# Performance work log

Hardware: AMD Instinct MI355X
Metric: run time of the kernel (lower is better)

The kernel has to match this reference:

```python
import jax, jax.numpy as jnp
import numpy as np

N = 10000
E = 320000


def spmm(edge_row, edge_col, edge_val, h):
    # out[i] = sum_{e: row[e]==i} val[e] * h[col[e]]  (sparse adjacency @ h)
    msgs = edge_val[:, None] * h[edge_col]          # [E, d]
    return jax.ops.segment_sum(msgs, edge_row, num_segments=N)


def setup_inputs() -> dict:
    key = jax.random.key(0)
    ks = jax.random.split(key, 8)
    x = jax.random.normal(ks[0], (N, 128), dtype=jnp.float32)
    edge_row = jax.random.randint(ks[1], (E,), 0, N, dtype=jnp.int32)
    edge_col = jax.random.randint(ks[2], (E,), 0, N, dtype=jnp.int32)
    edge_val = jax.random.uniform(ks[3], (E,), dtype=jnp.float32)
    # Xavier-uniform-ish init as in the torch module: U(-1/sqrt(fan_out), 1/sqrt(fan_out))
    def w(k, fi, fo):
        s = 1.0 / np.sqrt(fo)
        return jax.random.uniform(k, (fi, fo), minval=-s, maxval=s, dtype=jnp.float32)
    W0 = w(ks[4], 128, 128)
    W1 = w(ks[5], 128, 128)
    W2 = w(ks[6], 128, 64)
    Wb = w(ks[7], 64, 64)
    return {"x": x, "edge_row": edge_row, "edge_col": edge_col, "edge_val": edge_val,
            "W0": W0, "W1": W1, "W2": W2, "Wb": Wb}


def reference(x, edge_row, edge_col, edge_val, W0, W1, W2, Wb):
    h = x
    for W in (W0, W1, W2):
        h = jax.nn.elu(spmm(edge_row, edge_col, edge_val, h @ W))
        # dropout is inactive in eval mode (training=False)
    S = (Wb + Wb.T) * 0.5                          # symmetric [d, d]
    out = jax.nn.sigmoid(h @ (S @ h.T))            # [N, N]
    return out
```

## Files before the change

### kernel.cpp

```cpp
#include <hip/hip_runtime.h>
#include <hip/hip_bf16.h>
#include <math.h>

typedef short short8 __attribute__((ext_vector_type(8)));
typedef short short4v __attribute__((ext_vector_type(4)));
typedef float f32x4 __attribute__((ext_vector_type(4)));

__device__ inline void bsplit(float x, short& h, short& l) {
    __hip_bfloat16 hb = __float2bfloat16(x);
    float hf = __bfloat162float(hb);
    __hip_bfloat16 lb = __float2bfloat16(x - hf);
    h = *reinterpret_cast<short*>(&hb);
    l = *reinterpret_cast<short*>(&lb);
}


__global__ void zero_i32(int* __restrict__ p, int n) {
    int i = blockIdx.x * blockDim.x + threadIdx.x;
    if (i < n) p[i] = 0;
}

__global__ void hist_kernel(const int* __restrict__ row, int* __restrict__ hist, int E) {
    int i = blockIdx.x * blockDim.x + threadIdx.x;
    if (i < E) atomicAdd(&hist[row[i]], 1);
}

__global__ void scan_kernel(const int* __restrict__ hist, int* __restrict__ rowptr,
                            int* __restrict__ cursor, int n) {
    __shared__ int wsum[16];
    __shared__ int carry_s;
    int tid = threadIdx.x, lane = tid & 63, wid = tid >> 6;
    if (tid == 0) { carry_s = 0; rowptr[0] = 0; }
    __syncthreads();
    for (int base = 0; base < n; base += 1024) {
        int idx = base + tid;
        int v = (idx < n) ? hist[idx] : 0;
        int x = v;
#pragma unroll
        for (int d = 1; d < 64; d <<= 1) {
            int t = __shfl_up(x, d, 64);
            if (lane >= d) x += t;
        }
        if (lane == 63) wsum[wid] = x;
        __syncthreads();
        if (wid == 0) {
            int s = (lane < 16) ? wsum[lane] : 0;
#pragma unroll
            for (int d = 1; d < 16; d <<= 1) {
                int t = __shfl_up(s, d, 64);
                if (lane >= d) s += t;
            }
            if (lane < 16) wsum[lane] = s;
        }
        __syncthreads();
        int woff = (wid > 0) ? wsum[wid - 1] : 0;
        int inc = x + woff + carry_s;
        if (idx < n) {
            rowptr[idx + 1] = inc;
            cursor[idx] = inc - v;
        }
        __syncthreads();
        if (tid == 1023) carry_s = inc;
        __syncthreads();
    }
}

__global__ void scatter_kernel(const int* __restrict__ row, const int* __restrict__ col,
                               const float* __restrict__ val, int* __restrict__ cursor,
                               int* __restrict__ colsort, float* __restrict__ valsort, int E) {
    int i = blockIdx.x * blockDim.x + threadIdx.x;
    if (i < E) {
        int r = row[i];
        int p = atomicAdd(&cursor[r], 1);
        colsort[p] = col[i];
        valsort[p] = val[i];
    }
}

template <int K, int M>
__global__ void gemm_layer(const float* __restrict__ A, const float* __restrict__ W,
                           float* __restrict__ out, int n) {
    __shared__ float a[8 * K];
    int j = threadIdx.x;
    int row0 = blockIdx.x * 8;
    constexpr int K4 = K / 4;
    for (int idx = j; idx < 8 * K4; idx += M) {
        int r = idx / K4, k4 = idx % K4;
        float4 v = make_float4(0.f, 0.f, 0.f, 0.f);
        if (row0 + r < n) v = *reinterpret_cast<const float4*>(A + (long)(row0 + r) * K + k4 * 4);
        *reinterpret_cast<float4*>(a + r * K + k4 * 4) = v;
    }
    __syncthreads();
    float acc[8] = {0, 0, 0, 0, 0, 0, 0, 0};
#pragma unroll 8
    for (int k = 0; k < K; k++) {
        float w = W[k * M + j];
#pragma unroll
        for (int r = 0; r < 8; r++) acc[r] += a[r * K + k] * w;
    }
#pragma unroll
    for (int r = 0; r < 8; r++) {
        if (row0 + r < n) out[(long)(row0 + r) * M + j] = acc[r];
    }
}

__global__ void gemm_head(const float* __restrict__ A, const float* __restrict__ S,
                          short* __restrict__ Th, short* __restrict__ Tl, int n) {
    __shared__ float a[8 * 64];
    int j = threadIdx.x;
    int row0 = blockIdx.x * 8;
    for (int idx = j; idx < 8 * 16; idx += 64) {
        int r = idx >> 4, k4 = idx & 15;
        float4 v = make_float4(0.f, 0.f, 0.f, 0.f);
        if (row0 + r < n) v = *reinterpret_cast<const float4*>(A + (long)(row0 + r) * 64 + k4 * 4);
        *reinterpret_cast<float4*>(a + r * 64 + k4 * 4) = v;
    }
    __syncthreads();
    float acc[8] = {0, 0, 0, 0, 0, 0, 0, 0};
#pragma unroll 8
    for (int k = 0; k < 64; k++) {
        float w = S[k * 64 + j];
#pragma unroll
        for (int r = 0; r < 8; r++) acc[r] += a[r * 64 + k] * w;
    }
#pragma unroll
    for (int r = 0; r < 8; r++) {
        if (row0 + r < n) {
            short h, l;
            bsplit(acc[r], h, l);
            Th[(long)(row0 + r) * 64 + j] = h;
            Tl[(long)(row0 + r) * 64 + j] = l;
        }
    }
}

template <int D>
__global__ void spmm_elu_v2(const int* __restrict__ rowptr, const int* __restrict__ cols,
                            const float* __restrict__ vals, const float* __restrict__ hw,
                            float* __restrict__ out, int n) {
    constexpr int LPR = D / 4;
    constexpr int EPI = 64 / LPR;
    int wave = (blockIdx.x * blockDim.x + threadIdx.x) >> 6;
    int lane = threadIdx.x & 63;
    if (wave >= n) return;
    int sub = lane % LPR, grp = lane / LPR;
    int s = rowptr[wave], e = rowptr[wave + 1];
    float ax = 0.f, ay = 0.f, az = 0.f, aw = 0.f;
    int pe = s + grp;
    int c = 0; float v = 0.f;
    if (pe < e) { c = cols[pe]; v = vals[pe]; }
    for (int p = s; p < e; p += EPI) {
        int pn = p + EPI + grp;
        int cn = 0; float vn = 0.f;
        if (pn < e) { cn = cols[pn]; vn = vals[pn]; }
        float4 h4 = *reinterpret_cast<const float4*>(hw + (long)c * D + sub * 4);
        ax += v * h4.x; ay += v * h4.y; az += v * h4.z; aw += v * h4.w;
        c = cn; v = vn;
    }
#pragma unroll
    for (int m = LPR; m < 64; m <<= 1) {
        ax += __shfl_xor(ax, m, 64);
        ay += __shfl_xor(ay, m, 64);
        az += __shfl_xor(az, m, 64);
        aw += __shfl_xor(aw, m, 64);
    }
    if (grp == 0) {
        float4 o;
        o.x = ax > 0.f ? ax : (__expf(ax) - 1.f);
        o.y = ay > 0.f ? ay : (__expf(ay) - 1.f);
        o.z = az > 0.f ? az : (__expf(az) - 1.f);
        o.w = aw > 0.f ? aw : (__expf(aw) - 1.f);
        *reinterpret_cast<float4*>(out + (long)wave * D + sub * 4) = o;
    }
}

__global__ void spmm_elu_split64(const int* __restrict__ rowptr, const int* __restrict__ cols,
                                 const float* __restrict__ vals, const float* __restrict__ hw,
                                 float* __restrict__ h3, short* __restrict__ Hh,
                                 short* __restrict__ Hl, int n) {
    constexpr int D = 64, LPR = 16, EPI = 4;
    int wave = (blockIdx.x * blockDim.x + threadIdx.x) >> 6;
    int lane = threadIdx.x & 63;
    if (wave >= n) return;
    int sub = lane % LPR, grp = lane / LPR;
    int s = rowptr[wave], e = rowptr[wave + 1];
    float ax = 0.f, ay = 0.f, az = 0.f, aw = 0.f;
    int pe = s + grp;
    int c = 0; float v = 0.f;
    if (pe < e) { c = cols[pe]; v = vals[pe]; }
    for (int p = s; p < e; p += EPI) {
        int pn = p + EPI + grp;
        int cn = 0; float vn = 0.f;
        if (pn < e) { cn = cols[pn]; vn = vals[pn]; }
        float4 h4 = *reinterpret_cast<const float4*>(hw + (long)c * D + sub * 4);
        ax += v * h4.x; ay += v * h4.y; az += v * h4.z; aw += v * h4.w;
        c = cn; v = vn;
    }
#pragma unroll
    for (int m = LPR; m < 64; m <<= 1) {
        ax += __shfl_xor(ax, m, 64);
        ay += __shfl_xor(ay, m, 64);
        az += __shfl_xor(az, m, 64);
        aw += __shfl_xor(aw, m, 64);
    }
    if (grp == 0) {
        float4 o;
        o.x = ax > 0.f ? ax : (__expf(ax) - 1.f);
        o.y = ay > 0.f ? ay : (__expf(ay) - 1.f);
        o.z = az > 0.f ? az : (__expf(az) - 1.f);
        o.w = aw > 0.f ? aw : (__expf(aw) - 1.f);
        *reinterpret_cast<float4*>(h3 + (long)wave * D + sub * 4) = o;
        short4v hs, ls;
        short t0, t1, t2, t3, u0, u1, u2, u3;
        bsplit(o.x, t0, u0);
        bsplit(o.y, t1, u1);
        bsplit(o.z, t2, u2);
        bsplit(o.w, t3, u3);
        hs[0] = t0; hs[1] = t1; hs[2] = t2; hs[3] = t3;
        ls[0] = u0; ls[1] = u1; ls[2] = u2; ls[3] = u3;
        *reinterpret_cast<short4v*>(Hh + (long)wave * D + sub * 4) = hs;
        *reinterpret_cast<short4v*>(Hl + (long)wave * D + sub * 4) = ls;
    }
}

__global__ void sym_kernel(const float* __restrict__ Wb, float* __restrict__ S) {
    int i = blockIdx.x * blockDim.x + threadIdx.x;
    if (i < 64 * 64) {
        int r = i >> 6, c = i & 63;
        S[i] = 0.5f * (Wb[r * 64 + c] + Wb[c * 64 + r]);
    }
}

__global__ void pad_zero(short* __restrict__ Th, short* __restrict__ Tl,
                         short* __restrict__ Hh, short* __restrict__ Hl,
                         int startRow, int padRows) {
    int i = blockIdx.x * blockDim.x + threadIdx.x;
    int tot = padRows * 64;
    if (i < tot) {
        long off = (long)startRow * 64 + i;
        Th[off] = 0; Tl[off] = 0; Hh[off] = 0; Hl[off] = 0;
    }
}

__global__ __launch_bounds__(256) void final_mfma(
    const short* __restrict__ Th, const short* __restrict__ Tl,
    const short* __restrict__ Hh, const short* __restrict__ Hl,
    float* __restrict__ out, int n) {
    int tid = threadIdx.x;
    int wave = tid >> 6, lane = tid & 63;
    int row0 = blockIdx.y * 128 + (wave >> 1) * 64;
    int col0 = blockIdx.x * 128 + (wave & 1) * 64;
    int lrow = lane & 15;
    int koff = (lane >> 4) * 8;

    const short* ThB = Th + (long)(row0 + lrow) * 64 + koff;
    const short* TlB = Tl + (long)(row0 + lrow) * 64 + koff;
    const short* HhB = Hh + (long)(col0 + lrow) * 64 + koff;
    const short* HlB = Hl + (long)(col0 + lrow) * 64 + koff;

    f32x4 acc[4][4];
#pragma unroll
    for (int r = 0; r < 4; r++)
#pragma unroll
        for (int c = 0; c < 4; c++) acc[r][c] = (f32x4){0.f, 0.f, 0.f, 0.f};

#pragma unroll
    for (int ks = 0; ks < 2; ks++) {
        int kb = ks * 32;
        short8 ah[4], bh[4], al[4], bl[4];
#pragma unroll
        for (int r = 0; r < 4; r++) ah[r] = *reinterpret_cast<const short8*>(ThB + (long)(r * 16) * 64 + kb);
#pragma unroll
        for (int c = 0; c < 4; c++) bh[c] = *reinterpret_cast<const short8*>(HhB + (long)(c * 16) * 64 + kb);
#pragma unroll
        for (int r = 0; r < 4; r++) al[r] = *reinterpret_cast<const short8*>(TlB + (long)(r * 16) * 64 + kb);
#pragma unroll
        for (int c = 0; c < 4; c++) bl[c] = *reinterpret_cast<const short8*>(HlB + (long)(c * 16) * 64 + kb);

#pragma unroll
        for (int r = 0; r < 4; r++)
#pragma unroll
            for (int c = 0; c < 4; c++)
                acc[r][c] = __builtin_amdgcn_mfma_f32_16x16x32_bf16(ah[r], bh[c], acc[r][c], 0, 0, 0);
#pragma unroll
        for (int r = 0; r < 4; r++)
#pragma unroll
            for (int c = 0; c < 4; c++)
                acc[r][c] = __builtin_amdgcn_mfma_f32_16x16x32_bf16(ah[r], bl[c], acc[r][c], 0, 0, 0);
#pragma unroll
        for (int r = 0; r < 4; r++)
#pragma unroll
            for (int c = 0; c < 4; c++)
                acc[r][c] = __builtin_amdgcn_mfma_f32_16x16x32_bf16(al[r], bh[c], acc[r][c], 0, 0, 0);
    }

    int orow = (lane >> 4) * 4;
    bool full = (row0 + 64 <= n) && (col0 + 64 <= n);
    if (full) {
#pragma unroll
        for (int r = 0; r < 4; r++) {
#pragma unroll
            for (int q = 0; q < 4; q++) {
                long base = (long)(row0 + r * 16 + orow + q) * n + col0 + lrow;
#pragma unroll
                for (int c = 0; c < 4; c++) {
                    float x = acc[r][c][q];
                    out[base + c * 16] = __builtin_amdgcn_rcpf(1.f + __expf(-x));
                }
            }
        }
    } else {
#pragma unroll
        for (int r = 0; r < 4; r++) {
#pragma unroll
            for (int q = 0; q < 4; q++) {
                int i = row0 + r * 16 + orow + q;
                if (i < n) {
#pragma unroll
                    for (int c = 0; c < 4; c++) {
                        int j = col0 + c * 16 + lrow;
                        if (j < n) {
                            float x = acc[r][c][q];
                            out[(long)i * n + j] = __builtin_amdgcn_rcpf(1.f + __expf(-x));
                        }
                    }
                }
            }
        }
    }
}

extern "C" void kernel_launch(void* const* d_in, const int* in_sizes, int n_in,
                              void* d_out, int out_size, void* d_ws, size_t ws_size,
                              hipStream_t stream) {
    const float* x    = (const float*)d_in[0];
    const int*   erow = (const int*)d_in[1];
    const int*   ecol = (const int*)d_in[2];
    const float* eval = (const float*)d_in[3];
    const float* W0   = (const float*)d_in[4];
    const float* W1   = (const float*)d_in[5];
    const float* W2   = (const float*)d_in[6];
    const float* Wb   = (const float*)d_in[7];
    float* out = (float*)d_out;

    int N = in_sizes[0] / 128;
    int E = in_sizes[1];
    int G = (N + 127) / 128;
    int Npad = G * 128;

    char* w = (char*)d_ws;
    size_t off = 0;
    auto alloc = [&](size_t bytes) -> void* {
        void* p = w + off;
        off += (bytes + 255) & ~(size_t)255;
        return p;
    };
    float* bufA    = (float*)alloc((size_t)N * 128 * 4);
    float* bufB    = (float*)alloc((size_t)N * 128 * 4);
    float* h3      = (float*)alloc((size_t)N * 64 * 4);
    float* S       = (float*)alloc(64 * 64 * 4);
    int*   colsort = (int*)alloc((size_t)E * 4);
    float* valsort = (float*)alloc((size_t)E * 4);
    int*   rowptr  = (int*)alloc((size_t)(N + 1) * 4);
    int*   cursor  = (int*)alloc((size_t)N * 4);
    int*   hist    = (int*)alloc((size_t)N * 4);
    short* Th      = (short*)alloc((size_t)Npad * 64 * 2);
    short* Tl      = (short*)alloc((size_t)Npad * 64 * 2);
    short* Hh      = (short*)alloc((size_t)Npad * 64 * 2);
    short* Hl      = (short*)alloc((size_t)Npad * 64 * 2);

    zero_i32<<<(N + 255) / 256, 256, 0, stream>>>(hist, N);
    hist_kernel<<<(E + 255) / 256, 256, 0, stream>>>(erow, hist, E);
    scan_kernel<<<1, 1024, 0, stream>>>(hist, rowptr, cursor, N);
    scatter_kernel<<<(E + 255) / 256, 256, 0, stream>>>(erow, ecol, eval, cursor, colsort, valsort, E);

    int gb8 = (N + 7) / 8;
    gemm_layer<128, 128><<<gb8, 128, 0, stream>>>(x, W0, bufB, N);
    spmm_elu_v2<128><<<(N + 3) / 4, 256, 0, stream>>>(rowptr, colsort, valsort, bufB, bufA, N);
    gemm_layer<128, 128><<<gb8, 128, 0, stream>>>(bufA, W1, bufB, N);
    spmm_elu_v2<128><<<(N + 3) / 4, 256, 0, stream>>>(rowptr, colsort, valsort, bufB, bufA, N);
    gemm_layer<128, 64><<<gb8, 64, 0, stream>>>(bufA, W2, bufB, N);
    spmm_elu_split64<<<(N + 3) / 4, 256, 0, stream>>>(rowptr, colsort, valsort, bufB, h3, Hh, Hl, N);

    sym_kernel<<<16, 256, 0, stream>>>(Wb, S);
    gemm_head<<<gb8, 64, 0, stream>>>(h3, S, Th, Tl, N);

    int padRows = Npad - N;
    if (padRows > 0)
        pad_zero<<<(padRows * 64 + 255) / 256, 256, 0, stream>>>(Th, Tl, Hh, Hl, N, padRows);

    final_mfma<<<dim3(G, G), 256, 0, stream>>>(Th, Tl, Hh, Hl, out, N);
}
```

Measured before the change: 316.2 us.

## Split 128-wide SpMM into two column halves and remap final GEMM blocks per XCD

```diff
diff --git a/kernel.cpp b/kernel.cpp
--- a/kernel.cpp
+++ b/kernel.cpp
@@ -134,12 +134,10 @@
     }
 }
 
-template <int D>
-__global__ void spmm_elu_v2(const int* __restrict__ rowptr, const int* __restrict__ cols,
-                            const float* __restrict__ vals, const float* __restrict__ hw,
-                            float* __restrict__ out, int n) {
-    constexpr int LPR = D / 4;
-    constexpr int EPI = 64 / LPR;
+__global__ void spmm_elu_half(const int* __restrict__ rowptr, const int* __restrict__ cols,
+                              const float* __restrict__ vals, const float* __restrict__ hw,
+                              int tstride, float* __restrict__ out, int ostride, int n) {
+    constexpr int LPR = 16, EPI = 4;
     int wave = (blockIdx.x * blockDim.x + threadIdx.x) >> 6;
     int lane = threadIdx.x & 63;
     if (wave >= n) return;
@@ -153,7 +151,7 @@
         int pn = p + EPI + grp;
         int cn = 0; float vn = 0.f;
         if (pn < e) { cn = cols[pn]; vn = vals[pn]; }
-        float4 h4 = *reinterpret_cast<const float4*>(hw + (long)c * D + sub * 4);
+        float4 h4 = *reinterpret_cast<const float4*>(hw + (long)c * tstride + sub * 4);
         ax += v * h4.x; ay += v * h4.y; az += v * h4.z; aw += v * h4.w;
         c = cn; v = vn;
     }
@@ -170,7 +168,7 @@
         o.y = ay > 0.f ? ay : (__expf(ay) - 1.f);
         o.z = az > 0.f ? az : (__expf(az) - 1.f);
         o.w = aw > 0.f ? aw : (__expf(aw) - 1.f);
-        *reinterpret_cast<float4*>(out + (long)wave * D + sub * 4) = o;
+        *reinterpret_cast<float4*>(out + (long)wave * ostride + sub * 4) = o;
     }
 }
 
@@ -245,11 +243,18 @@
 __global__ __launch_bounds__(256) void final_mfma(
     const short* __restrict__ Th, const short* __restrict__ Tl,
     const short* __restrict__ Hh, const short* __restrict__ Hl,
-    float* __restrict__ out, int n) {
+    float* __restrict__ out, int n, int G, int ypx) {
+    int bid = blockIdx.x;
+    int xcd = bid & 7;
+    int s4 = bid >> 3;
+    int by = xcd * ypx + s4 % ypx;
+    int bx = s4 / ypx;
+    if (by >= G) return;
+
     int tid = threadIdx.x;
     int wave = tid >> 6, lane = tid & 63;
-    int row0 = blockIdx.y * 128 + (wave >> 1) * 64;
-    int col0 = blockIdx.x * 128 + (wave & 1) * 64;
+    int row0 = by * 128 + (wave >> 1) * 64;
+    int col0 = bx * 128 + (wave & 1) * 64;
     int lrow = lane & 15;
     int koff = (lane >> 4) * 8;
 
@@ -375,12 +380,15 @@
     scatter_kernel<<<(E + 255) / 256, 256, 0, stream>>>(erow, ecol, eval, cursor, colsort, valsort, E);
 
     int gb8 = (N + 7) / 8;
+    int spmmG = (N + 3) / 4;
     gemm_layer<128, 128><<<gb8, 128, 0, stream>>>(x, W0, bufB, N);
-    spmm_elu_v2<128><<<(N + 3) / 4, 256, 0, stream>>>(rowptr, colsort, valsort, bufB, bufA, N);
+    spmm_elu_half<<<spmmG, 256, 0, stream>>>(rowptr, colsort, valsort, bufB, 128, bufA, 128, N);
+    spmm_elu_half<<<spmmG, 256, 0, stream>>>(rowptr, colsort, valsort, bufB + 64, 128, bufA + 64, 128, N);
     gemm_layer<128, 128><<<gb8, 128, 0, stream>>>(bufA, W1, bufB, N);
-    spmm_elu_v2<128><<<(N + 3) / 4, 256, 0, stream>>>(rowptr, colsort, valsort, bufB, bufA, N);
+    spmm_elu_half<<<spmmG, 256, 0, stream>>>(rowptr, colsort, valsort, bufB, 128, bufA, 128, N);
+    spmm_elu_half<<<spmmG, 256, 0, stream>>>(rowptr, colsort, valsort, bufB + 64, 128, bufA + 64, 128, N);
     gemm_layer<128, 64><<<gb8, 64, 0, stream>>>(bufA, W2, bufB, N);
-    spmm_elu_split64<<<(N + 3) / 4, 256, 0, stream>>>(rowptr, colsort, valsort, bufB, h3, Hh, Hl, N);
+    spmm_elu_split64<<<spmmG, 256, 0, stream>>>(rowptr, colsort, valsort, bufB, h3, Hh, Hl, N);
 
     sym_kernel<<<16, 256, 0, stream>>>(Wb, S);
     gemm_head<<<gb8, 64, 0, stream>>>(h3, S, Th, Tl, N);
@@ -389,5 +397,7 @@
     if (padRows > 0)
         pad_zero<<<(padRows * 64 + 255) / 256, 256, 0, stream>>>(Th, Tl, Hh, Hl, N, padRows);
 
-    final_mfma<<<dim3(G, G), 256, 0, stream>>>(Th, Tl, Hh, Hl, out, N);
-}
+    int ypx = (G + 7) / 8;
+    int nwg = 8 * ypx * G;
+    final_mfma<<<nwg, 256, 0, stream>>>(Th, Tl, Hh, Hl, out, N, G, ypx);
+}
```

Result: no change. 316.6 us (+0.1%).
